# Kernel tuning notes

Hardware: AMD Instinct MI355X
Metric: run time of the kernel (lower is better)

## Reference

```python
import jax, jax.numpy as jnp
import numpy as np

B, C, N, M_MODES, EMB = 8, 64, 2048, 32, 256
MFREQ = 2 * M_MODES * (2 * M_MODES - 1)  # 4032
SCALE = 1.0 / (C * C)


def setup_inputs() -> dict:
    key = jax.random.key(0)
    ks = jax.random.split(key, 16)
    d = {
        "x": jax.random.normal(ks[0], (B, C, N), jnp.float32),
        "emb": jax.random.normal(ks[1], (B, EMB), jnp.float32),
        "Vf_re": jax.random.normal(ks[2], (MFREQ, N), jnp.float32),
        "Vf_im": jax.random.normal(ks[3], (MFREQ, N), jnp.float32),
        "Vi_re": jax.random.normal(ks[4], (N, MFREQ), jnp.float32),
        "Vi_im": jax.random.normal(ks[5], (N, MFREQ), jnp.float32),
        "w1_re": SCALE * jax.random.uniform(ks[6], (C, C, M_MODES, M_MODES), jnp.float32),
        "w1_im": SCALE * jax.random.uniform(ks[7], (C, C, M_MODES, M_MODES), jnp.float32),
        "w2_re": SCALE * jax.random.uniform(ks[8], (C, C, M_MODES, M_MODES), jnp.float32),
        "w2_im": SCALE * jax.random.uniform(ks[9], (C, C, M_MODES, M_MODES), jnp.float32),
        "m1_re": SCALE * jax.random.uniform(ks[10], (1, M_MODES, M_MODES, EMB), jnp.float32),
        "m1_im": SCALE * jax.random.uniform(ks[11], (1, M_MODES, M_MODES, EMB), jnp.float32),
        "m2_re": SCALE * jax.random.uniform(ks[12], (1, M_MODES, M_MODES, EMB), jnp.float32),
        "m2_im": SCALE * jax.random.uniform(ks[13], (1, M_MODES, M_MODES, EMB), jnp.float32),
    }
    return d


def _spectral_conv(x, emb, Vf, Vi, w1, w2, mod1, mod2):
    m = M_MODES
    # nuft.forward: [B,N,C] complex -> [B,MFREQ,C]
    xc = jnp.transpose(x, (0, 2, 1)).astype(jnp.complex64)
    x_nfft = jnp.einsum('mn,bnc->bmc', Vf, xc)
    # [B,C,2m,2m-1]
    x_ft = jnp.transpose(x_nfft, (0, 2, 1)).reshape(x.shape[0], C, 2 * m, 2 * m - 1)
    embc = emb.astype(jnp.complex64)[:, None, None, :]  # [B,1,1,EMB]
    phi1 = jnp.sum(mod1 * embc, axis=-1)  # [B,m,m]
    phi2 = jnp.sum(mod2 * embc, axis=-1)
    out1 = jnp.einsum('bixy,ioxy->boxy', x_ft[:, :, :m, :m], w1)
    out2 = jnp.einsum('bixy,ioxy->boxy', x_ft[:, :, -m:, :m], w2)
    mod1b = phi1[:, None, :, :] * out1
    mod2b = phi2[:, None, :, :] * out2
    out_ft = jnp.concatenate([mod1b, mod2b], axis=2)  # [B,C,2m,m]
    xf = out_ft.reshape(x.shape[0], C, 2 * m * m)
    # Hermitian-symmetry reconstruction: flip over mode AND channel dims, conj
    xf2 = jnp.conj(jnp.flip(xf[..., 2 * m:], axis=(-2, -1)))
    xf = jnp.concatenate([xf, xf2], axis=-1)  # [B,C,MFREQ]
    xf = jnp.transpose(xf, (0, 2, 1))  # [B,MFREQ,C]
    out = jnp.einsum('nm,bmc->bnc', Vi, xf)  # nuft.inverse -> [B,N,C]
    out = jnp.transpose(out, (0, 2, 1)) / N * 2
    return out.real


def reference(x, emb, Vf_re, Vf_im, Vi_re, Vi_im, w1_re, w1_im, w2_re, w2_im, m1_re, m1_im, m2_re, m2_im):
    Vf = Vf_re + 1j * Vf_im
    Vi = Vi_re + 1j * Vi_im
    w1 = w1_re + 1j * w1_im
    w2 = w2_re + 1j * w2_im
    mod1 = m1_re + 1j * m1_im
    mod2 = m2_re + 1j * m2_im
    return _spectral_conv(x, emb, Vf, Vi, w1, w2, mod1, mod2)
```

## Files before the change

### kernel.cpp

```cpp
#include <hip/hip_runtime.h>

#define BB    8
#define CC    64
#define NN    2048
#define GG    2048
#define MFREQ 4032

typedef __attribute__((ext_vector_type(4))) float f32x4;
typedef __attribute__((ext_vector_type(8))) short bf16x8;

static __device__ __forceinline__ unsigned short f2bf(float f) {
    union { float f; unsigned u; } v; v.f = f;
    unsigned r = v.u + 0x7fff + ((v.u >> 16) & 1);
    return (unsigned short)(r >> 16);
}

static __device__ __forceinline__ unsigned int pk2(float lo, float hi) {
    return (unsigned int)f2bf(lo) | ((unsigned int)f2bf(hi) << 16);
}

#define ASYNC_COPY16(gp, lp)                                                        \
    __builtin_amdgcn_global_load_lds(                                               \
        (const __attribute__((address_space(1))) unsigned int*)(gp),                \
        (__attribute__((address_space(3))) unsigned int*)(lp), 16, 0, 0)

static __device__ __forceinline__ void decode_unit(int uid,
        const float* __restrict__ vf_re, const float* __restrict__ vf_im,
        const float* __restrict__ x,
        const float* __restrict__ vi_re, const float* __restrict__ vi_im,
        unsigned short* __restrict__ af, unsigned short* __restrict__ xb,
        unsigned short* __restrict__ mi,
        const float*& pa, const float*& pb, unsigned short*& dst, int& mode) {
    if (uid < 1048576) {
        int m = uid >> 8;
        int q8 = (uid & 255) * 8;
        int g = m & 2047;
        int f = (g >> 5) * 63 + (g & 31);
        const float* src = (m < 2048 ? vf_re : vf_im) + (size_t)f * 2048 + q8;
        pa = src; pb = src + 4; dst = af + (size_t)m * 2048 + q8; mode = 0;
    } else if (uid < 1179648) {
        int v = uid - 1048576;
        int q8 = v * 8;
        pa = x + q8; pb = x + q8 + 4; dst = xb + q8; mode = 0;
    } else {
        int v = uid - 1179648;
        int n = v >> 10;
        int q8 = (v & 1023) * 8;
        int region = q8 >> 11;
        int off = q8 & 2047;
        dst = mi + (size_t)n * 8192 + q8;
        if (region == 0) {
            pa = vi_re + (size_t)n * MFREQ + off; pb = pa + 4; mode = 0;
        } else if (region == 1) {
            pa = vi_im + (size_t)n * MFREQ + off; pb = pa + 4; mode = 1;
        } else {
            const float* src = (region == 2 ? vi_re : vi_im) + (size_t)n * MFREQ;
            if (off < 64) { pa = src; pb = src; mode = 3; }
            else { pa = src + 4092 - off; pb = src + 4088 - off; mode = 2; }
        }
    }
}

static __device__ __forceinline__ uint4 pack_unit(float4 a, float4 b, int mode) {
    uint4 o;
    if (mode == 3) { o.x = o.y = o.z = o.w = 0u; return o; }
    if (mode == 2) {
        o.x = pk2(a.w, a.z); o.y = pk2(a.y, a.x);
        o.z = pk2(b.w, b.z); o.w = pk2(b.y, b.x);
    } else if (mode == 1) {
        o.x = pk2(-a.x, -a.y); o.y = pk2(-a.z, -a.w);
        o.z = pk2(-b.x, -b.y); o.w = pk2(-b.z, -b.w);
    } else {
        o.x = pk2(a.x, a.y); o.y = pk2(a.z, a.w);
        o.z = pk2(b.x, b.y); o.w = pk2(b.z, b.w);
    }
    return o;
}

__global__ __launch_bounds__(256) void prep_all(const float* __restrict__ vf_re,
                                                const float* __restrict__ vf_im,
                                                const float* __restrict__ x,
                                                const float* __restrict__ vi_re,
                                                const float* __restrict__ vi_im,
                                                const float* __restrict__ w1_re,
                                                const float* __restrict__ w1_im,
                                                const float* __restrict__ w2_re,
                                                const float* __restrict__ w2_im,
                                                const float* __restrict__ m1_re,
                                                const float* __restrict__ m1_im,
                                                const float* __restrict__ m2_re,
                                                const float* __restrict__ m2_im,
                                                const float* __restrict__ emb,
                                                unsigned short* __restrict__ af,
                                                unsigned short* __restrict__ xb,
                                                unsigned short* __restrict__ mi,
                                                unsigned int* __restrict__ wt,
                                                float* __restrict__ phi_re,
                                                float* __restrict__ phi_im) {
    __shared__ float sre[32][33];
    __shared__ float sim[32][33];
    __shared__ float sr4[4], si4[4];
    int blk = blockIdx.x;
    int t = threadIdx.x;

    if (blk < 1280) {
        const int STRIDE = 1280 * 256;
        int uid0 = blk * 256 + t;
        const float *pa0, *pb0; unsigned short* d0; int md0;
        decode_unit(uid0, vf_re, vf_im, x, vi_re, vi_im, af, xb, mi, pa0, pb0, d0, md0);
        float4 A0 = *(const float4*)pa0;
        float4 B0 = *(const float4*)pb0;
        #pragma unroll
        for (int i = 1; i <= 10; ++i) {
            const float *pa1 = pa0, *pb1 = pb0; unsigned short* d1 = d0; int md1 = md0;
            float4 A1 = A0, B1 = B0;
            if (i < 10) {
                decode_unit(uid0 + i * STRIDE, vf_re, vf_im, x, vi_re, vi_im,
                            af, xb, mi, pa1, pb1, d1, md1);
                A1 = *(const float4*)pa1;
                B1 = *(const float4*)pb1;
            }
            uint4 o = pack_unit(A0, B0, md0);
            *(uint4*)d0 = o;
            A0 = A1; B0 = B1; d0 = d1; md0 = md1;
            pa0 = pa1; pb0 = pb1;
        }
    } else if (blk < 9472) {
        int bi = blk - 1280;
        int wsel = bi >> 12;
        int bj = bi & 4095;
        int io0 = (bj >> 5) * 32;
        int xy0 = (bj & 31) * 32;
        const float* wre = wsel ? w2_re : w1_re;
        const float* wim = wsel ? w2_im : w1_im;
        int r = t >> 3, c4 = (t & 7) * 4;
        float4 a = *(const float4*)(wre + (size_t)(io0 + r) * 1024 + xy0 + c4);
        float4 b = *(const float4*)(wim + (size_t)(io0 + r) * 1024 + xy0 + c4);
        sre[r][c4 + 0] = a.x; sre[r][c4 + 1] = a.y; sre[r][c4 + 2] = a.z; sre[r][c4 + 3] = a.w;
        sim[r][c4 + 0] = b.x; sim[r][c4 + 1] = b.y; sim[r][c4 + 2] = b.z; sim[r][c4 + 3] = b.w;
        __syncthreads();
        int gr = t >> 3, ic4 = (t & 7) * 4;
        uint4 o;
        o.x = (unsigned int)f2bf(sre[ic4 + 0][gr]) | ((unsigned int)f2bf(sim[ic4 + 0][gr]) << 16);
        o.y = (unsigned int)f2bf(sre[ic4 + 1][gr]) | ((unsigned int)f2bf(sim[ic4 + 1][gr]) << 16);
        o.z = (unsigned int)f2bf(sre[ic4 + 2][gr]) | ((unsigned int)f2bf(sim[ic4 + 2][gr]) << 16);
        o.w = (unsigned int)f2bf(sre[ic4 + 3][gr]) | ((unsigned int)f2bf(sim[ic4 + 3][gr]) << 16);
        int g = xy0 + gr + wsel * 1024;
        *(uint4*)(wt + (size_t)g * 4096 + io0 + ic4) = o;
    } else {
        int g = blk - 9472, e = t;
        int xy = g & 1023;
        const float* mr = (g < 1024 ? m1_re : m2_re) + xy * 256;
        const float* mp = (g < 1024 ? m1_im : m2_im) + xy * 256;
        float vr = mr[e], vi = mp[e];
        for (int bb = 0; bb < 8; ++bb) {
            float em = emb[bb * 256 + e];
            float pr = vr * em, pi = vi * em;
            for (int s = 32; s > 0; s >>= 1) { pr += __shfl_down(pr, s); pi += __shfl_down(pi, s); }
            int wid = e >> 6;
            if ((e & 63) == 0) { sr4[wid] = pr; si4[wid] = pi; }
            __syncthreads();
            if (e == 0) {
                phi_re[bb * 2048 + g] = sr4[0] + sr4[1] + sr4[2] + sr4[3];
                phi_im[bb * 2048 + g] = si4[0] + si4[1] + si4[2] + si4[3];
            }
            __syncthreads();
        }
    }
}

template<int TM>
__global__ __launch_bounds__(256, 2) void gemm_sk(const unsigned short* __restrict__ A,
                                                  const unsigned short* __restrict__ Bm,
                                                  float* __restrict__ P,
                                                  int M, int N, int K, int Kper, int ilv) {
    constexpr int FI = TM / 32;
    __shared__ unsigned short As[TM * 64];
    __shared__ unsigned short Bs[TM * 64];
    int t = threadIdx.x;
    int lane = t & 63, w = t >> 6;

    unsigned nx = gridDim.x, ny = gridDim.y;
    unsigned nwg = nx * ny * gridDim.z;
    unsigned orig = (blockIdx.z * ny + blockIdx.y) * nx + blockIdx.x;
    unsigned cpx = nwg >> 3;
    unsigned wid = (orig & 7) * cpx + (orig >> 3);
    unsigned bx = wid % nx; unsigned rem = wid / nx;
    unsigned by = rem % ny; unsigned bz = rem / ny;

    int m0 = by * TM, n0 = bx * TM;
    int z = bz;
    int kbase = z * Kper;
    int wm = (w >> 1) * (TM / 2), wn = (w & 1) * (TM / 2);
    int lr = lane & 15, quad = lane >> 4;
    int rsub = lane >> 3, slot = lane & 7;

    f32x4 acc[FI][FI] = {};

    for (int kk = kbase; kk < kbase + Kper; kk += 64) {
        __syncthreads();
        #pragma unroll
        for (int l = 0; l < FI; ++l) {
            int r = (w * FI + l) * 8 + rsub;
            int c = slot ^ (r & 7);
            ASYNC_COPY16(A + (size_t)(m0 + r) * K + kk + c * 8, As + r * 64 + slot * 8);
            ASYNC_COPY16(Bm + (size_t)(n0 + r) * K + kk + c * 8, Bs + r * 64 + slot * 8);
        }
        __syncthreads();
        #pragma unroll
        for (int ks = 0; ks < 2; ++ks) {
            bf16x8 af[FI], bfr[FI];
            #pragma unroll
            for (int i = 0; i < FI; ++i) {
                int row = wm + i * 16 + lr;
                int q = (ks * 4 + quad) ^ (row & 7);
                af[i] = *(const bf16x8*)(As + row * 64 + q * 8);
                int rowb = wn + i * 16 + lr;
                int qb = (ks * 4 + quad) ^ (rowb & 7);
                bfr[i] = *(const bf16x8*)(Bs + rowb * 64 + qb * 8);
            }
            #pragma unroll
            for (int i = 0; i < FI; ++i)
            #pragma unroll
            for (int j = 0; j < FI; ++j)
                acc[i][j] = __builtin_amdgcn_mfma_f32_16x16x32_bf16(af[i], bfr[j], acc[i][j], 0, 0, 0);
        }
    }
    float* Pz = P + (size_t)z * M * N;
    size_t rstride = ilv ? 1024 : (size_t)N;
    #pragma unroll
    for (int i = 0; i < FI; ++i)
    #pragma unroll
    for (int j = 0; j < FI; ++j) {
        int rr = m0 + wm + i * 16 + quad * 4;
        int cc = n0 + wn + j * 16 + lr;
        size_t base = ilv ? ((size_t)(rr & 2047) * 1024 + cc * 2 + (rr >> 11))
                          : ((size_t)rr * N + cc);
        float* cp = Pz + base;
        f32x4 v = acc[i][j];
        cp[0]           = v.x;
        cp[rstride]     = v.y;
        cp[2 * rstride] = v.z;
        cp[3 * rstride] = v.w;
    }
}

__global__ __launch_bounds__(256) void reduce_k(const float* __restrict__ P,
                                                float* __restrict__ out,
                                                int S, size_t elems, float alpha) {
    size_t idx = ((size_t)blockIdx.x * 256 + threadIdx.x) * 4;
    float4 s = *(const float4*)(P + idx);
    for (int zz = 1; zz < S; ++zz) {
        float4 v = *(const float4*)(P + (size_t)zz * elems + idx);
        s.x += v.x; s.y += v.y; s.z += v.z; s.w += v.w;
    }
    s.x *= alpha; s.y *= alpha; s.z *= alpha; s.w *= alpha;
    *(float4*)(out + idx) = s;
}

__global__ __launch_bounds__(256, 4) void middle_k(const float* __restrict__ O1,
                                                   const unsigned int* __restrict__ wt,
                                                   const float* __restrict__ phi_re,
                                                   const float* __restrict__ phi_im,
                                                   unsigned short* __restrict__ Yt) {
    __shared__ unsigned int sW[2][4096];
    __shared__ float sInc[2][1024];
    int t = threadIdx.x;
    int g0 = blockIdx.x * 2;
    int b = t >> 5, p = t & 31;

    #pragma unroll
    for (int gt = 0; gt < 2; ++gt) {
        int g = g0 + gt;
        #pragma unroll
        for (int j = 0; j < 4; ++j)
            ASYNC_COPY16(wt + (size_t)g * 4096 + (j * 256 + t) * 4, &sW[gt][(j * 256 + t) * 4]);
        ASYNC_COPY16(O1 + (size_t)g * 1024 + t * 4, &sInc[gt][t * 4]);
    }
    __syncthreads();

    unsigned short reA[2][2], imA[2][2];

    #pragma unroll
    for (int gt = 0; gt < 2; ++gt) {
        int g = g0 + gt;
        float ar0 = 0.f, ai0 = 0.f, ar1 = 0.f, ai1 = 0.f;
        const float2* incp = (const float2*)sInc[gt] + b * 64;
        const unsigned int* wp = sW[gt] + 2 * p;
        #pragma unroll 8
        for (int i = 0; i < 64; ++i) {
            float2 a = incp[i];
            uint2 uu = *(const uint2*)(wp + i * 64);
            float w0r = __uint_as_float(uu.x << 16);
            float w0i = __uint_as_float(uu.x & 0xffff0000u);
            float w1r = __uint_as_float(uu.y << 16);
            float w1i = __uint_as_float(uu.y & 0xffff0000u);
            ar0 += a.x * w0r - a.y * w0i;  ai0 += a.x * w0i + a.y * w0r;
            ar1 += a.x * w1r - a.y * w1i;  ai1 += a.x * w1i + a.y * w1r;
        }
        float pr = phi_re[b * 2048 + g], pi = phi_im[b * 2048 + g];
        reA[0][gt] = f2bf(pr * ar0 - pi * ai0);
        imA[0][gt] = f2bf(pr * ai0 + pi * ar0);
        reA[1][gt] = f2bf(pr * ar1 - pi * ai1);
        imA[1][gt] = f2bf(pr * ai1 + pi * ar1);
    }

    #pragma unroll
    for (int ch = 0; ch < 2; ++ch) {
        int c = 2 * p + ch;
        size_t r0 = (size_t)(b * 64 + c) * 8192;
        size_t rf = (size_t)(b * 64 + 63 - c) * 8192;
        unsigned int ure = (unsigned int)reA[ch][0] | ((unsigned int)reA[ch][1] << 16);
        unsigned int uim = (unsigned int)imA[ch][0] | ((unsigned int)imA[ch][1] << 16);
        *(unsigned int*)(Yt + r0 + g0)        = ure;
        *(unsigned int*)(Yt + r0 + 2048 + g0) = uim;
        *(unsigned int*)(Yt + rf + 4096 + g0) = ure;
        *(unsigned int*)(Yt + rf + 6144 + g0) = uim;
    }
}

extern "C" void kernel_launch(void* const* d_in, const int* in_sizes, int n_in,
                              void* d_out, int out_size, void* d_ws, size_t ws_size,
                              hipStream_t stream) {
    const float* x     = (const float*)d_in[0];
    const float* emb   = (const float*)d_in[1];
    const float* vf_re = (const float*)d_in[2];
    const float* vf_im = (const float*)d_in[3];
    const float* vi_re = (const float*)d_in[4];
    const float* vi_im = (const float*)d_in[5];
    const float* w1_re = (const float*)d_in[6];
    const float* w1_im = (const float*)d_in[7];
    const float* w2_re = (const float*)d_in[8];
    const float* w2_im = (const float*)d_in[9];
    const float* m1_re = (const float*)d_in[10];
    const float* m1_im = (const float*)d_in[11];
    const float* m2_re = (const float*)d_in[12];
    const float* m2_im = (const float*)d_in[13];

    char* ws = (char*)d_ws;
    unsigned short* Af = (unsigned short*)(ws);
    unsigned short* Xb = (unsigned short*)(ws + 16777216);
    unsigned short* Mi = (unsigned short*)(ws + 18874368);
    unsigned int*   Wt = (unsigned int*)(ws + 52428800);
    float*          O1 = (float*)(ws + 85983232);
    float*       PhiRe = (float*)(ws + 94371840);
    float*       PhiIm = (float*)(ws + 94437376);
    unsigned short* Yt = (unsigned short*)(ws + 94502912);
    float*          P  = (float*)(ws + 102891520);
    float* out = (float*)d_out;

    prep_all<<<11520, 256, 0, stream>>>(vf_re, vf_im, x, vi_re, vi_im,
                                        w1_re, w1_im, w2_re, w2_im,
                                        m1_re, m1_im, m2_re, m2_im, emb,
                                        Af, Xb, Mi, Wt, PhiRe, PhiIm);

    gemm_sk<64><<<dim3(8, 64, 1), 256, 0, stream>>>(Af, Xb, O1, 4096, 512, 2048, 2048, 1);

    middle_k<<<1024, 256, 0, stream>>>(O1, Wt, PhiRe, PhiIm, Yt);

    gemm_sk<128><<<dim3(16, 4, 8), 256, 0, stream>>>(Yt, Mi, P, 512, 2048, 8192, 1024, 0);
    reduce_k<<<1024, 256, 0, stream>>>(P, out, 8, (size_t)512 * 2048, 1.0f / 1024.0f);
}
```

Baseline: 318.2 us.

## Double-buffer LDS tiles in split-K GEMM and drop XCD workgroup remap

Switches the GEMM's LDS staging to two buffers so the async global-to-LDS copies for the next K tile are issued before computing on the current tile, with one barrier per iteration. This aims to overlap global load latency with MFMA work. It also removes the workgroup-ID swizzle that grouped blocks per XCD, using plain blockIdx mapping instead, which may hurt L2 locality. Doubling LDS use can lower occupancy under the launch bound of two blocks per CU.

```diff
diff --git a/kernel.cpp b/kernel.cpp
--- a/kernel.cpp
+++ b/kernel.cpp
@@ -175,38 +175,35 @@
                                                   float* __restrict__ P,
                                                   int M, int N, int K, int Kper, int ilv) {
     constexpr int FI = TM / 32;
-    __shared__ unsigned short As[TM * 64];
-    __shared__ unsigned short Bs[TM * 64];
+    __shared__ unsigned short As[2][TM * 64];
+    __shared__ unsigned short Bs[2][TM * 64];
     int t = threadIdx.x;
     int lane = t & 63, w = t >> 6;
-
-    unsigned nx = gridDim.x, ny = gridDim.y;
-    unsigned nwg = nx * ny * gridDim.z;
-    unsigned orig = (blockIdx.z * ny + blockIdx.y) * nx + blockIdx.x;
-    unsigned cpx = nwg >> 3;
-    unsigned wid = (orig & 7) * cpx + (orig >> 3);
-    unsigned bx = wid % nx; unsigned rem = wid / nx;
-    unsigned by = rem % ny; unsigned bz = rem / ny;
-
-    int m0 = by * TM, n0 = bx * TM;
-    int z = bz;
+    int m0 = blockIdx.y * TM, n0 = blockIdx.x * TM;
+    int z = blockIdx.z;
     int kbase = z * Kper;
     int wm = (w >> 1) * (TM / 2), wn = (w & 1) * (TM / 2);
     int lr = lane & 15, quad = lane >> 4;
     int rsub = lane >> 3, slot = lane & 7;
 
-    f32x4 acc[FI][FI] = {};
-
-    for (int kk = kbase; kk < kbase + Kper; kk += 64) {
-        __syncthreads();
+    auto stage = [&](int kk, int buf) {
         #pragma unroll
         for (int l = 0; l < FI; ++l) {
             int r = (w * FI + l) * 8 + rsub;
             int c = slot ^ (r & 7);
-            ASYNC_COPY16(A + (size_t)(m0 + r) * K + kk + c * 8, As + r * 64 + slot * 8);
-            ASYNC_COPY16(Bm + (size_t)(n0 + r) * K + kk + c * 8, Bs + r * 64 + slot * 8);
-        }
-        __syncthreads();
+            ASYNC_COPY16(A + (size_t)(m0 + r) * K + kk + c * 8, &As[buf][r * 64 + slot * 8]);
+            ASYNC_COPY16(Bm + (size_t)(n0 + r) * K + kk + c * 8, &Bs[buf][r * 64 + slot * 8]);
+        }
+    };
+
+    f32x4 acc[FI][FI] = {};
+
+    int nt = Kper >> 6;
+    stage(kbase, 0);
+    __syncthreads();
+    for (int tt = 0; tt < nt; ++tt) {
+        int cur = tt & 1;
+        if (tt + 1 < nt) stage(kbase + (tt + 1) * 64, cur ^ 1);
         #pragma unroll
         for (int ks = 0; ks < 2; ++ks) {
             bf16x8 af[FI], bfr[FI];
@@ -214,10 +211,10 @@
             for (int i = 0; i < FI; ++i) {
                 int row = wm + i * 16 + lr;
                 int q = (ks * 4 + quad) ^ (row & 7);
-                af[i] = *(const bf16x8*)(As + row * 64 + q * 8);
+                af[i] = *(const bf16x8*)(&As[cur][row * 64 + q * 8]);
                 int rowb = wn + i * 16 + lr;
                 int qb = (ks * 4 + quad) ^ (rowb & 7);
-                bfr[i] = *(const bf16x8*)(Bs + rowb * 64 + qb * 8);
+                bfr[i] = *(const bf16x8*)(&Bs[cur][rowb * 64 + qb * 8]);
             }
             #pragma unroll
             for (int i = 0; i < FI; ++i)
@@ -225,7 +222,9 @@
             for (int j = 0; j < FI; ++j)
                 acc[i][j] = __builtin_amdgcn_mfma_f32_16x16x32_bf16(af[i], bfr[j], acc[i][j], 0, 0, 0);
         }
-    }
+        __syncthreads();
+    }
+
     float* Pz = P + (size_t)z * M * N;
     size_t rstride = ilv ? 1024 : (size_t)N;
     #pragma unroll
```

Result: no change. 323.6 us (+1.7%).

## Drop weight pre-transpose, read fp32 weights directly in mode-mixing kernel, reorder O1 layout

Applied to the files above, without the earlier changes.

Removes the bf16 transpose/pack of the w1/w2 spectral weights from the prep kernel. The mode-mixing kernel now reads the fp32 weights straight from global memory with coalesced float4 loads along the mode dimension. To make that work, the first GEMM writes O1 with modes contiguous per channel row, and each block handles 32 modes × 32 output channels × 2 batches. The XCD-aware block swizzle in the GEMM is also removed. This cuts a 64 MB weight write-then-read pass but doubles the weight bytes read per use (fp32 instead of bf16), and weights are re-read for each batch pair.

```diff
diff --git a/kernel.cpp b/kernel.cpp
--- a/kernel.cpp
+++ b/kernel.cpp
@@ -17,6 +17,22 @@
 
 static __device__ __forceinline__ unsigned int pk2(float lo, float hi) {
     return (unsigned int)f2bf(lo) | ((unsigned int)f2bf(hi) << 16);
+}
+
+static __device__ __forceinline__ uint4 pack_unit(float4 a, float4 b, int mode) {
+    uint4 o;
+    if (mode == 3) { o.x = o.y = o.z = o.w = 0u; return o; }
+    if (mode == 2) {
+        o.x = pk2(a.w, a.z); o.y = pk2(a.y, a.x);
+        o.z = pk2(b.w, b.z); o.w = pk2(b.y, b.x);
+    } else if (mode == 1) {
+        o.x = pk2(-a.x, -a.y); o.y = pk2(-a.z, -a.w);
+        o.z = pk2(-b.x, -b.y); o.w = pk2(-b.z, -b.w);
+    } else {
+        o.x = pk2(a.x, a.y); o.y = pk2(a.z, a.w);
+        o.z = pk2(b.x, b.y); o.w = pk2(b.z, b.w);
+    }
+    return o;
 }
 
 #define ASYNC_COPY16(gp, lp)                                                        \
@@ -61,31 +77,11 @@
     }
 }
 
-static __device__ __forceinline__ uint4 pack_unit(float4 a, float4 b, int mode) {
-    uint4 o;
-    if (mode == 3) { o.x = o.y = o.z = o.w = 0u; return o; }
-    if (mode == 2) {
-        o.x = pk2(a.w, a.z); o.y = pk2(a.y, a.x);
-        o.z = pk2(b.w, b.z); o.w = pk2(b.y, b.x);
-    } else if (mode == 1) {
-        o.x = pk2(-a.x, -a.y); o.y = pk2(-a.z, -a.w);
-        o.z = pk2(-b.x, -b.y); o.w = pk2(-b.z, -b.w);
-    } else {
-        o.x = pk2(a.x, a.y); o.y = pk2(a.z, a.w);
-        o.z = pk2(b.x, b.y); o.w = pk2(b.z, b.w);
-    }
-    return o;
-}
-
 __global__ __launch_bounds__(256) void prep_all(const float* __restrict__ vf_re,
                                                 const float* __restrict__ vf_im,
                                                 const float* __restrict__ x,
                                                 const float* __restrict__ vi_re,
                                                 const float* __restrict__ vi_im,
-                                                const float* __restrict__ w1_re,
-                                                const float* __restrict__ w1_im,
-                                                const float* __restrict__ w2_re,
-                                                const float* __restrict__ w2_im,
                                                 const float* __restrict__ m1_re,
                                                 const float* __restrict__ m1_im,
                                                 const float* __restrict__ m2_re,
@@ -94,11 +90,8 @@
                                                 unsigned short* __restrict__ af,
                                                 unsigned short* __restrict__ xb,
                                                 unsigned short* __restrict__ mi,
-                                                unsigned int* __restrict__ wt,
                                                 float* __restrict__ phi_re,
                                                 float* __restrict__ phi_im) {
-    __shared__ float sre[32][33];
-    __shared__ float sim[32][33];
     __shared__ float sr4[4], si4[4];
     int blk = blockIdx.x;
     int t = threadIdx.x;
@@ -125,30 +118,8 @@
             A0 = A1; B0 = B1; d0 = d1; md0 = md1;
             pa0 = pa1; pb0 = pb1;
         }
-    } else if (blk < 9472) {
-        int bi = blk - 1280;
-        int wsel = bi >> 12;
-        int bj = bi & 4095;
-        int io0 = (bj >> 5) * 32;
-        int xy0 = (bj & 31) * 32;
-        const float* wre = wsel ? w2_re : w1_re;
-        const float* wim = wsel ? w2_im : w1_im;
-        int r = t >> 3, c4 = (t & 7) * 4;
-        float4 a = *(const float4*)(wre + (size_t)(io0 + r) * 1024 + xy0 + c4);
-        float4 b = *(const float4*)(wim + (size_t)(io0 + r) * 1024 + xy0 + c4);
-        sre[r][c4 + 0] = a.x; sre[r][c4 + 1] = a.y; sre[r][c4 + 2] = a.z; sre[r][c4 + 3] = a.w;
-        sim[r][c4 + 0] = b.x; sim[r][c4 + 1] = b.y; sim[r][c4 + 2] = b.z; sim[r][c4 + 3] = b.w;
-        __syncthreads();
-        int gr = t >> 3, ic4 = (t & 7) * 4;
-        uint4 o;
-        o.x = (unsigned int)f2bf(sre[ic4 + 0][gr]) | ((unsigned int)f2bf(sim[ic4 + 0][gr]) << 16);
-        o.y = (unsigned int)f2bf(sre[ic4 + 1][gr]) | ((unsigned int)f2bf(sim[ic4 + 1][gr]) << 16);
-        o.z = (unsigned int)f2bf(sre[ic4 + 2][gr]) | ((unsigned int)f2bf(sim[ic4 + 2][gr]) << 16);
-        o.w = (unsigned int)f2bf(sre[ic4 + 3][gr]) | ((unsigned int)f2bf(sim[ic4 + 3][gr]) << 16);
-        int g = xy0 + gr + wsel * 1024;
-        *(uint4*)(wt + (size_t)g * 4096 + io0 + ic4) = o;
     } else {
-        int g = blk - 9472, e = t;
+        int g = blk - 1280, e = t;
         int xy = g & 1023;
         const float* mr = (g < 1024 ? m1_re : m2_re) + xy * 256;
         const float* mp = (g < 1024 ? m1_im : m2_im) + xy * 256;
@@ -179,17 +150,8 @@
     __shared__ unsigned short Bs[TM * 64];
     int t = threadIdx.x;
     int lane = t & 63, w = t >> 6;
-
-    unsigned nx = gridDim.x, ny = gridDim.y;
-    unsigned nwg = nx * ny * gridDim.z;
-    unsigned orig = (blockIdx.z * ny + blockIdx.y) * nx + blockIdx.x;
-    unsigned cpx = nwg >> 3;
-    unsigned wid = (orig & 7) * cpx + (orig >> 3);
-    unsigned bx = wid % nx; unsigned rem = wid / nx;
-    unsigned by = rem % ny; unsigned bz = rem / ny;
-
-    int m0 = by * TM, n0 = bx * TM;
-    int z = bz;
+    int m0 = blockIdx.y * TM, n0 = blockIdx.x * TM;
+    int z = blockIdx.z;
     int kbase = z * Kper;
     int wm = (w >> 1) * (TM / 2), wn = (w & 1) * (TM / 2);
     int lr = lane & 15, quad = lane >> 4;
@@ -227,14 +189,14 @@
         }
     }
     float* Pz = P + (size_t)z * M * N;
-    size_t rstride = ilv ? 1024 : (size_t)N;
+    size_t rstride = ilv ? 2 : (size_t)N;
     #pragma unroll
     for (int i = 0; i < FI; ++i)
     #pragma unroll
     for (int j = 0; j < FI; ++j) {
         int rr = m0 + wm + i * 16 + quad * 4;
         int cc = n0 + wn + j * 16 + lr;
-        size_t base = ilv ? ((size_t)(rr & 2047) * 1024 + cc * 2 + (rr >> 11))
+        size_t base = ilv ? ((size_t)cc * 4096 + (size_t)(rr & 2047) * 2 + (rr >> 11))
                           : ((size_t)rr * N + cc);
         float* cp = Pz + base;
         f32x4 v = acc[i][j];
@@ -258,64 +220,80 @@
     *(float4*)(out + idx) = s;
 }
 
-__global__ __launch_bounds__(256, 4) void middle_k(const float* __restrict__ O1,
-                                                   const unsigned int* __restrict__ wt,
-                                                   const float* __restrict__ phi_re,
-                                                   const float* __restrict__ phi_im,
-                                                   unsigned short* __restrict__ Yt) {
-    __shared__ unsigned int sW[2][4096];
-    __shared__ float sInc[2][1024];
+__global__ __launch_bounds__(256) void middle_k2(const float* __restrict__ O1,
+                                                 const float* __restrict__ w1_re,
+                                                 const float* __restrict__ w1_im,
+                                                 const float* __restrict__ w2_re,
+                                                 const float* __restrict__ w2_im,
+                                                 const float* __restrict__ phi_re,
+                                                 const float* __restrict__ phi_im,
+                                                 unsigned short* __restrict__ Yt) {
+    __shared__ float sO1[128 * 64];
     int t = threadIdx.x;
-    int g0 = blockIdx.x * 2;
-    int b = t >> 5, p = t & 31;
+    int bx = blockIdx.x;
+    int g0 = (bx & 63) * 32;
+    int o0 = ((bx >> 6) & 1) * 32;
+    int b0 = (bx >> 7) * 2;
+    const float* wre = (g0 < 1024 ? w1_re : w2_re);
+    const float* wim = (g0 < 1024 ? w1_im : w2_im);
+    int xyb = g0 & 1023;
 
     #pragma unroll
-    for (int gt = 0; gt < 2; ++gt) {
-        int g = g0 + gt;
+    for (int s = 0; s < 8; ++s) {
+        int idx = s * 256 + t;
+        int row = idx >> 4;
+        int off = (idx & 15) * 4;
+        ASYNC_COPY16(O1 + (size_t)(b0 * 64 + row) * 4096 + g0 * 2 + off,
+                     sO1 + row * 64 + off);
+    }
+    __syncthreads();
+
+    int ol = t >> 3, gq = t & 7;
+    int o = o0 + ol;
+    float accr[2][4] = {}, acci[2][4] = {};
+
+    #pragma unroll 4
+    for (int i = 0; i < 64; ++i) {
+        size_t wrow = (size_t)(i * 64 + o) * 1024 + xyb + gq * 4;
+        float4 wr = *(const float4*)(wre + wrow);
+        float4 wi = *(const float4*)(wim + wrow);
         #pragma unroll
-        for (int j = 0; j < 4; ++j)
-            ASYNC_COPY16(wt + (size_t)g * 4096 + (j * 256 + t) * 4, &sW[gt][(j * 256 + t) * 4]);
-        ASYNC_COPY16(O1 + (size_t)g * 1024 + t * 4, &sInc[gt][t * 4]);
-    }
-    __syncthreads();
-
-    unsigned short reA[2][2], imA[2][2];
-
+        for (int b = 0; b < 2; ++b) {
+            const float* op = sO1 + (b * 64 + i) * 64 + gq * 8;
+            float4 oa = *(const float4*)op;
+            float4 ob = *(const float4*)(op + 4);
+            accr[b][0] += wr.x * oa.x - wi.x * oa.y;
+            acci[b][0] += wr.x * oa.y + wi.x * oa.x;
+            accr[b][1] += wr.y * oa.z - wi.y * oa.w;
+            acci[b][1] += wr.y * oa.w + wi.y * oa.z;
+            accr[b][2] += wr.z * ob.x - wi.z * ob.y;
+            acci[b][2] += wr.z * ob.y + wi.z * ob.x;
+            accr[b][3] += wr.w * ob.z - wi.w * ob.w;
+            acci[b][3] += wr.w * ob.w + wi.w * ob.z;
+        }
+    }
+
+    int g4 = g0 + gq * 4;
     #pragma unroll
-    for (int gt = 0; gt < 2; ++gt) {
-        int g = g0 + gt;
-        float ar0 = 0.f, ai0 = 0.f, ar1 = 0.f, ai1 = 0.f;
-        const float2* incp = (const float2*)sInc[gt] + b * 64;
-        const unsigned int* wp = sW[gt] + 2 * p;
-        #pragma unroll 8
-        for (int i = 0; i < 64; ++i) {
-            float2 a = incp[i];
-            uint2 uu = *(const uint2*)(wp + i * 64);
-            float w0r = __uint_as_float(uu.x << 16);
-            float w0i = __uint_as_float(uu.x & 0xffff0000u);
-            float w1r = __uint_as_float(uu.y << 16);
-            float w1i = __uint_as_float(uu.y & 0xffff0000u);
-            ar0 += a.x * w0r - a.y * w0i;  ai0 += a.x * w0i + a.y * w0r;
-            ar1 += a.x * w1r - a.y * w1i;  ai1 += a.x * w1i + a.y * w1r;
-        }
-        float pr = phi_re[b * 2048 + g], pi = phi_im[b * 2048 + g];
-        reA[0][gt] = f2bf(pr * ar0 - pi * ai0);
-        imA[0][gt] = f2bf(pr * ai0 + pi * ar0);
-        reA[1][gt] = f2bf(pr * ar1 - pi * ai1);
-        imA[1][gt] = f2bf(pr * ai1 + pi * ar1);
-    }
-
-    #pragma unroll
-    for (int ch = 0; ch < 2; ++ch) {
-        int c = 2 * p + ch;
-        size_t r0 = (size_t)(b * 64 + c) * 8192;
-        size_t rf = (size_t)(b * 64 + 63 - c) * 8192;
-        unsigned int ure = (unsigned int)reA[ch][0] | ((unsigned int)reA[ch][1] << 16);
-        unsigned int uim = (unsigned int)imA[ch][0] | ((unsigned int)imA[ch][1] << 16);
-        *(unsigned int*)(Yt + r0 + g0)        = ure;
-        *(unsigned int*)(Yt + r0 + 2048 + g0) = uim;
-        *(unsigned int*)(Yt + rf + 4096 + g0) = ure;
-        *(unsigned int*)(Yt + rf + 6144 + g0) = uim;
+    for (int b = 0; b < 2; ++b) {
+        int bb = b0 + b;
+        float4 pr = *(const float4*)(phi_re + bb * 2048 + g4);
+        float4 pi = *(const float4*)(phi_im + bb * 2048 + g4);
+        ushort4 vre, vim;
+        vre.x = f2bf(pr.x * accr[b][0] - pi.x * acci[b][0]);
+        vim.x = f2bf(pr.x * acci[b][0] + pi.x * accr[b][0]);
+        vre.y = f2bf(pr.y * accr[b][1] - pi.y * acci[b][1]);
+        vim.y = f2bf(pr.y * acci[b][1] + pi.y * accr[b][1]);
+        vre.z = f2bf(pr.z * accr[b][2] - pi.z * acci[b][2]);
+        vim.z = f2bf(pr.z * acci[b][2] + pi.z * accr[b][2]);
+        vre.w = f2bf(pr.w * accr[b][3] - pi.w * acci[b][3]);
+        vim.w = f2bf(pr.w * acci[b][3] + pi.w * accr[b][3]);
+        size_t r0 = (size_t)(bb * 64 + o) * 8192;
+        size_t rf = (size_t)(bb * 64 + 63 - o) * 8192;
+        *(ushort4*)(Yt + r0 + g4)        = vre;
+        *(ushort4*)(Yt + r0 + 2048 + g4) = vim;
+        *(ushort4*)(Yt + rf + 4096 + g4) = vre;
+        *(ushort4*)(Yt + rf + 6144 + g4) = vim;
     }
 }
 
@@ -341,7 +319,6 @@
     unsigned short* Af = (unsigned short*)(ws);
     unsigned short* Xb = (unsigned short*)(ws + 16777216);
     unsigned short* Mi = (unsigned short*)(ws + 18874368);
-    unsigned int*   Wt = (unsigned int*)(ws + 52428800);
     float*          O1 = (float*)(ws + 85983232);
     float*       PhiRe = (float*)(ws + 94371840);
     float*       PhiIm = (float*)(ws + 94437376);
@@ -349,14 +326,14 @@
     float*          P  = (float*)(ws + 102891520);
     float* out = (float*)d_out;
 
-    prep_all<<<11520, 256, 0, stream>>>(vf_re, vf_im, x, vi_re, vi_im,
-                                        w1_re, w1_im, w2_re, w2_im,
-                                        m1_re, m1_im, m2_re, m2_im, emb,
-                                        Af, Xb, Mi, Wt, PhiRe, PhiIm);
+    prep_all<<<3328, 256, 0, stream>>>(vf_re, vf_im, x, vi_re, vi_im,
+                                       m1_re, m1_im, m2_re, m2_im, emb,
+                                       Af, Xb, Mi, PhiRe, PhiIm);
 
     gemm_sk<64><<<dim3(8, 64, 1), 256, 0, stream>>>(Af, Xb, O1, 4096, 512, 2048, 2048, 1);
 
-    middle_k<<<1024, 256, 0, stream>>>(O1, Wt, PhiRe, PhiIm, Yt);
+    middle_k2<<<512, 256, 0, stream>>>(O1, w1_re, w1_im, w2_re, w2_im,
+                                       PhiRe, PhiIm, Yt);
 
     gemm_sk<128><<<dim3(16, 4, 8), 256, 0, stream>>>(Yt, Mi, P, 512, 2048, 8192, 1024, 0);
     reduce_k<<<1024, 256, 0, stream>>>(P, out, 8, (size_t)512 * 2048, 1.0f / 1024.0f);
```

After: 314.0 us. Within noise of the previous version (-1.3%).
